# Kernel optimization log

Hardware: AMD Instinct MI355X
Metric: run time of the kernel (lower is better)

Reference implementation:

```python
import jax, jax.numpy as jnp
import numpy as np

N = 50000      # nodes
E = 800000     # edges (before self-loops)
F_IN = 128     # in_dim
H = 8          # heads
C = 16         # out_dim per head
NEG_SLOPE = 0.2
EPS = 1e-5


def setup_inputs() -> dict:
    key = jax.random.key(0)
    ks = jax.random.split(key, 8)
    x = jax.random.normal(ks[0], (N, F_IN), dtype=jnp.float32)
    edge_index = jax.random.randint(ks[1], (2, E), 0, N, dtype=jnp.int64)
    # GAT linear weight (xavier-ish scale), stored as [F_IN, H*C]
    W_gat = jax.random.normal(ks[2], (F_IN, H * C), dtype=jnp.float32) * 0.1
    att_src = jax.random.normal(ks[3], (H, C), dtype=jnp.float32) * 0.1
    att_dst = jax.random.normal(ks[4], (H, C), dtype=jnp.float32) * 0.1
    bias_gat = jnp.zeros((H * C,), dtype=jnp.float32)
    W_skip = jax.random.normal(ks[5], (F_IN, H * C), dtype=jnp.float32) * 0.1
    gamma = jnp.ones((H * C,), dtype=jnp.float32)
    beta = jnp.zeros((H * C,), dtype=jnp.float32)
    return {"x": x, "edge_index": edge_index, "W_gat": W_gat,
            "att_src": att_src, "att_dst": att_dst, "bias_gat": bias_gat,
            "W_skip": W_skip, "gamma": gamma, "beta": beta}


def reference(x, edge_index, W_gat, att_src, att_dst, bias_gat, W_skip, gamma, beta):
    # PyG GATConv default: add self-loops
    loop = jnp.arange(N, dtype=edge_index.dtype)
    src = jnp.concatenate([edge_index[0], loop])  # [E+N]
    dst = jnp.concatenate([edge_index[1], loop])  # [E+N]

    h = (x @ W_gat).reshape(N, H, C)              # [N,H,C]
    a_src = jnp.sum(h * att_src, axis=-1)          # [N,H]
    a_dst = jnp.sum(h * att_dst, axis=-1)          # [N,H]

    e = jax.nn.leaky_relu(a_src[src] + a_dst[dst], NEG_SLOPE)   # [E+N,H]
    # segment softmax over destination nodes
    e_max = jax.ops.segment_max(e, dst, num_segments=N)         # [N,H]
    e_exp = jnp.exp(e - e_max[dst])
    denom = jax.ops.segment_sum(e_exp, dst, num_segments=N)     # [N,H]
    alpha = e_exp / denom[dst]                                   # [E+N,H]

    msg = alpha[:, :, None] * h[src]                             # [E+N,H,C]
    gat_out = jax.ops.segment_sum(msg, dst, num_segments=N)     # [N,H,C]
    gat_out = gat_out.reshape(N, H * C) + bias_gat

    skip_out = x @ W_skip                                        # [N,H*C]
    z = gat_out + 0.1 * skip_out

    mu = jnp.mean(z, axis=-1, keepdims=True)
    var = jnp.mean((z - mu) ** 2, axis=-1, keepdims=True)
    z = (z - mu) * jax.lax.rsqrt(var + EPS) * gamma + beta
    return jax.nn.elu(z)  # dropout is identity in eval mode
```

## Files before the change

### kernel.cpp

```cpp
#include <hip/hip_runtime.h>
#include <hip/hip_bf16.h>

#define N_NODES 50000
#define N_EDGES 800000
#define F_IN    128
#define HC      128
#define NR      8
#define RSZ     6250
#define NCH     32
#define CHSZ    25000
#define NP      50048

#define LOG2E   1.4426950408889634f

typedef __attribute__((ext_vector_type(8))) short bf16x8;
typedef __attribute__((ext_vector_type(4))) float f32x4;

__device__ __forceinline__ float bf2f(unsigned int u16) {
    return __uint_as_float(u16 << 16);
}
__device__ __forceinline__ unsigned int f2bf2(float lo, float hi) {
    unsigned int r;
    asm("v_cvt_pk_bf16_f32 %0, %1, %2" : "=v"(r) : "v"(lo), "v"(hi));
    return r;
}
__device__ __forceinline__ float exp2_hw(float x) {
    float r;
    asm("v_exp_f32 %0, %1" : "=v"(r) : "v"(x));
    return r;
}

__device__ __forceinline__ void linear_block(
    int lin, int tid, int* smem,
    const float* __restrict__ x, const unsigned short* __restrict__ Bfrag,
    const float* __restrict__ att_s, const float* __restrict__ att_d,
    const float* __restrict__ bias,
    unsigned short* __restrict__ h_bf, unsigned int* __restrict__ z0b,
    float* __restrict__ a_src, float* __restrict__ a_dst)
{
    unsigned short* sA = (unsigned short*)smem;
    const int lane = tid & 63;
    const int w = tid >> 6;
    const int nbase = lin * 64;

#pragma unroll
    for (int it = 0; it < 4; it++) {
        const int p = it * 256 + tid;
        const int node = p >> 4;
        const int kg = p & 15;
        const int gn = nbase + node;
        float v[8];
        if (gn < N_NODES) {
            float4 u0 = *(const float4*)(x + (size_t)gn * F_IN + kg * 8);
            float4 u1 = *(const float4*)(x + (size_t)gn * F_IN + kg * 8 + 4);
            v[0] = u0.x; v[1] = u0.y; v[2] = u0.z; v[3] = u0.w;
            v[4] = u1.x; v[5] = u1.y; v[6] = u1.z; v[7] = u1.w;
        } else {
#pragma unroll
            for (int j = 0; j < 8; j++) v[j] = 0.f;
        }
        const int mt = node >> 4, lm = node & 15;
        const int kq = kg >> 2, quad = kg & 3;
        uint4 pk;
        pk.x = f2bf2(v[0], v[1]);
        pk.y = f2bf2(v[2], v[3]);
        pk.z = f2bf2(v[4], v[5]);
        pk.w = f2bf2(v[6], v[7]);
        *(uint4*)(sA + ((size_t)((mt * 4 + kq) * 64 + quad * 16 + lm)) * 8) = pk;
    }
    __syncthreads();

    const bf16x8* Bf = (const bf16x8*)Bfrag;
    f32x4 acc[4][4];
#pragma unroll
    for (int mt = 0; mt < 4; mt++)
#pragma unroll
        for (int nt = 0; nt < 4; nt++)
            acc[mt][nt] = (f32x4){0.f, 0.f, 0.f, 0.f};

#pragma unroll
    for (int kq = 0; kq < 4; kq++) {
        bf16x8 aF[4], bF[4];
#pragma unroll
        for (int nt = 0; nt < 4; nt++)
            bF[nt] = Bf[(size_t)(((w * 4 + nt) * 4 + kq) * 64 + lane)];
#pragma unroll
        for (int mt = 0; mt < 4; mt++)
            aF[mt] = *(const bf16x8*)(sA + ((size_t)((mt * 4 + kq) * 64 + lane)) * 8);
#pragma unroll
        for (int mt = 0; mt < 4; mt++)
#pragma unroll
            for (int nt = 0; nt < 4; nt++)
                acc[mt][nt] = __builtin_amdgcn_mfma_f32_16x16x32_bf16(
                    aF[mt], bF[nt], acc[mt][nt], 0, 0, 0);
    }

    __syncthreads();

    const int row4 = (lane >> 4) * 4;
    const int cl = lane & 15;
    unsigned int* hls = (unsigned int*)smem;

    if (w < 2) {
#pragma unroll
        for (int mt = 0; mt < 4; mt++) {
#pragma unroll
            for (int nt = 0; nt < 4; nt++) {
                const int cc = w * 64 + nt * 16 + cl;
                f32x4 d = acc[mt][nt];
#pragma unroll
                for (int rr = 0; rr < 4; rr++) {
                    const float oth = __shfl_xor(d[rr], 1);
                    const unsigned int pk = f2bf2(d[rr], oth);
                    if ((cl & 1) == 0) {
                        const int nl = mt * 16 + row4 + rr;
                        hls[nl * 68 + (cc >> 1)] = pk;
                    }
                }
            }
        }
    } else {
#pragma unroll
        for (int mt = 0; mt < 4; mt++) {
#pragma unroll
            for (int nt = 0; nt < 4; nt++) {
                const int cz = (w - 2) * 64 + nt * 16 + cl;
                f32x4 d = acc[mt][nt];
                const float bv = bias[cz];
#pragma unroll
                for (int rr = 0; rr < 4; rr++) {
                    const int gn = nbase + mt * 16 + row4 + rr;
                    const float val = 0.1f * d[rr] + bv;
                    const float oth = __shfl_xor(val, 1);
                    const unsigned int pk = f2bf2(val, oth);
                    if ((cl & 1) == 0 && gn < N_NODES)
                        z0b[(size_t)gn * 64 + (cz >> 1)] = pk;
                }
            }
        }
    }
    __syncthreads();

    {
        const int row = tid >> 2, q = tid & 3;
        const int gn = nbase + row;
        if (gn < N_NODES) {
            const unsigned int* hr = hls + row * 68 + q * 16;
            uint4 v0 = *(const uint4*)(hr);
            uint4 v1 = *(const uint4*)(hr + 4);
            uint4 v2 = *(const uint4*)(hr + 8);
            uint4 v3 = *(const uint4*)(hr + 12);
            uint4* hout = (uint4*)((unsigned int*)h_bf + (size_t)gn * 64 + q * 16);
            hout[0] = v0; hout[1] = v1; hout[2] = v2; hout[3] = v3;

            const unsigned int u[16] = {v0.x, v0.y, v0.z, v0.w,
                                        v1.x, v1.y, v1.z, v1.w,
                                        v2.x, v2.y, v2.z, v2.w,
                                        v3.x, v3.y, v3.z, v3.w};
            const int c0 = q * 32;
            const float4* as4 = (const float4*)(att_s + c0);
            const float4* ad4 = (const float4*)(att_d + c0);
            float ds0 = 0.f, dd0 = 0.f, ds1 = 0.f, dd1 = 0.f;
#pragma unroll
            for (int j = 0; j < 4; j++) {
                const float4 sa = as4[j], da = ad4[j];
                float l0 = bf2f(u[2 * j] & 0xffffu),     h0v = bf2f(u[2 * j] >> 16);
                float l1 = bf2f(u[2 * j + 1] & 0xffffu), h1v = bf2f(u[2 * j + 1] >> 16);
                ds0 += l0 * sa.x + h0v * sa.y + l1 * sa.z + h1v * sa.w;
                dd0 += l0 * da.x + h0v * da.y + l1 * da.z + h1v * da.w;
                const float4 sb = as4[4 + j], db = ad4[4 + j];
                float l2 = bf2f(u[8 + 2 * j] & 0xffffu),     h2v = bf2f(u[8 + 2 * j] >> 16);
                float l3 = bf2f(u[8 + 2 * j + 1] & 0xffffu), h3v = bf2f(u[8 + 2 * j + 1] >> 16);
                ds1 += l2 * sb.x + h2v * sb.y + l3 * sb.z + h3v * sb.w;
                dd1 += l2 * db.x + h2v * db.y + l3 * db.z + h3v * db.w;
            }
            const int hh = 2 * q;
            a_src[gn * 8 + hh]     = ds0 * LOG2E;
            a_src[gn * 8 + hh + 1] = ds1 * LOG2E;
            a_dst[gn * 8 + hh]     = dd0 * LOG2E;
            a_dst[gn * 8 + hh + 1] = dd1 * LOG2E;
        }
    }
}

__global__ __launch_bounds__(256) void k_pack(
    const float* __restrict__ Wg, const float* __restrict__ Ws,
    unsigned short* __restrict__ Bfrag)
{
    const int g = blockIdx.x * 256 + threadIdx.x;
    if (g < 4096) {
        const int lane = g & 63;
        const int kq = (g >> 6) & 3;
        const int nt = g >> 8;
        const int cc = nt * 16 + (lane & 15);
        const int kbase = kq * 32 + (lane >> 4) * 8;
        const float* Wsel = (cc < 128) ? (Wg + cc) : (Ws + cc - 128);
        unsigned int pk[4];
#pragma unroll
        for (int p = 0; p < 4; p++) {
            const float v0 = Wsel[(size_t)(kbase + 2 * p) * HC];
            const float v1 = Wsel[(size_t)(kbase + 2 * p + 1) * HC];
            pk[p] = f2bf2(v0, v1);
        }
        *(uint4*)(Bfrag + (size_t)g * 8) = make_uint4(pk[0], pk[1], pk[2], pk[3]);
    }
}

__global__ __launch_bounds__(256) void k_hl(
    const int* __restrict__ dst, int* __restrict__ part,
    const float* __restrict__ x, const unsigned short* __restrict__ Bfrag,
    const float* __restrict__ att_s, const float* __restrict__ att_d,
    const float* __restrict__ bias,
    unsigned short* __restrict__ h_bf, unsigned int* __restrict__ z0b,
    float* __restrict__ a_src, float* __restrict__ a_dst)
{
    __shared__ __align__(16) int smem[RSZ];
    const int bid = blockIdx.x;
    const int tid = threadIdx.x;
    if (bid < 256) {
        const int r = bid & 7, c = bid >> 3;
        const int nb = r * RSZ;
        for (int i = tid; i < RSZ; i += 256) smem[i] = 0;
        __syncthreads();
        const int4* d4 = (const int4*)(dst + c * CHSZ);
        for (int i = tid; i < CHSZ / 4; i += 256) {
            const int4 v = d4[i];
            int b;
            b = v.x - nb; if ((unsigned)b < (unsigned)RSZ) atomicAdd(&smem[b], 1);
            b = v.y - nb; if ((unsigned)b < (unsigned)RSZ) atomicAdd(&smem[b], 1);
            b = v.z - nb; if ((unsigned)b < (unsigned)RSZ) atomicAdd(&smem[b], 1);
            b = v.w - nb; if ((unsigned)b < (unsigned)RSZ) atomicAdd(&smem[b], 1);
        }
        __syncthreads();
        for (int i = tid; i < RSZ; i += 256)
            part[(size_t)c * NP + nb + i] = smem[i];
        return;
    }
    linear_block(bid - 256, tid, smem, x, Bfrag, att_s, att_d, bias,
                 h_bf, z0b, a_src, a_dst);
}

__global__ __launch_bounds__(256) void k_sl(
    int* __restrict__ part, int* __restrict__ counts,
    int* __restrict__ row_start, int* __restrict__ bsum,
    const float* __restrict__ x, const unsigned short* __restrict__ Bfrag,
    const float* __restrict__ att_s, const float* __restrict__ att_d,
    const float* __restrict__ bias,
    unsigned short* __restrict__ h_bf, unsigned int* __restrict__ z0b,
    float* __restrict__ a_src, float* __restrict__ a_dst)
{
    __shared__ __align__(16) int smem[RSZ];
    const int bid = blockIdx.x;
    const int tid = threadIdx.x;
    if (bid < 49) {
        int* s = smem;
        const int base = bid * 1024 + tid * 4;
        int v[4]; int t = 0;
#pragma unroll
        for (int j = 0; j < 4; j++) {
            const int idx = base + j;
            if (idx < N_NODES) {
                int run = 0;
#pragma unroll
                for (int c = 0; c < NCH; c++) {
                    int* p = part + (size_t)c * NP + idx;
                    const int q = *p;
                    *p = run;
                    run += q;
                }
                counts[idx] = run;
                v[j] = run + 1;
            } else v[j] = 0;
            t += v[j];
        }
        s[tid] = t;
        __syncthreads();
        for (int off = 1; off < 256; off <<= 1) {
            int add = (tid >= off) ? s[tid - off] : 0;
            __syncthreads();
            s[tid] += add;
            __syncthreads();
        }
        int excl = s[tid] - t;
#pragma unroll
        for (int j = 0; j < 4; j++) {
            const int idx = base + j;
            if (idx < N_NODES) row_start[idx] = excl;
            excl += v[j];
        }
        if (tid == 255) bsum[bid] = s[255];
        return;
    }
    linear_block(260 + (bid - 49), tid, smem, x, Bfrag, att_s, att_d, bias,
                 h_bf, z0b, a_src, a_dst);
}

__global__ __launch_bounds__(256) void k_lf(
    const int* __restrict__ src, const int* __restrict__ dst,
    const int* __restrict__ row_start, const int* __restrict__ part,
    const int* __restrict__ bsum, const int* __restrict__ counts,
    int* __restrict__ row_fin, int* __restrict__ csr,
    const float* __restrict__ x, const unsigned short* __restrict__ Bfrag,
    const float* __restrict__ att_s, const float* __restrict__ att_d,
    const float* __restrict__ bias,
    unsigned short* __restrict__ h_bf, unsigned int* __restrict__ z0b,
    float* __restrict__ a_src, float* __restrict__ a_dst)
{
    __shared__ __align__(16) int smem[RSZ];
    __shared__ int pbsum[64];
    const int bid = blockIdx.x;
    const int tid = threadIdx.x;
    int lin;
    if (bid < 512) {
        const int c = bid >> 4, pos = bid & 15;
        if (pos < 8) {
            const int r = pos;
            const int nb = r * RSZ;
            if (tid < 64) {
                const int val = (tid < 49) ? bsum[tid] : 0;
                int v = val;
#pragma unroll
                for (int off = 1; off < 64; off <<= 1) {
                    const int u = __shfl_up(v, off);
                    if (tid >= off) v += u;
                }
                pbsum[tid] = v - val;
            }
            __syncthreads();
            if (c == 0) {
                for (int b = tid; b < RSZ; b += 256) {
                    const int idx = nb + b;
                    const int rsf = row_start[idx] + pbsum[idx >> 10];
                    smem[b] = rsf + part[(size_t)c * NP + idx];
                    row_fin[idx] = rsf;
                    csr[rsf + counts[idx]] = idx;
                }
            } else {
                for (int b = tid; b < RSZ; b += 256) {
                    const int idx = nb + b;
                    smem[b] = row_start[idx] + pbsum[idx >> 10]
                            + part[(size_t)c * NP + idx];
                }
            }
            __syncthreads();
            const int4* d4 = (const int4*)(dst + c * CHSZ);
            const int4* s4 = (const int4*)(src + c * CHSZ);
            for (int i = tid; i < CHSZ / 4; i += 256) {
                const int4 dv = d4[i];
                const int4 sv = s4[i];
                int b;
                b = dv.x - nb; if ((unsigned)b < (unsigned)RSZ) csr[atomicAdd(&smem[b], 1)] = sv.x;
                b = dv.y - nb; if ((unsigned)b < (unsigned)RSZ) csr[atomicAdd(&smem[b], 1)] = sv.y;
                b = dv.z - nb; if ((unsigned)b < (unsigned)RSZ) csr[atomicAdd(&smem[b], 1)] = sv.z;
                b = dv.w - nb; if ((unsigned)b < (unsigned)RSZ) csr[atomicAdd(&smem[b], 1)] = sv.w;
            }
            return;
        }
        lin = 521 + c * 8 + (pos - 8);
    } else {
        lin = 777 + (bid - 512);
    }
    linear_block(lin, tid, smem, x, Bfrag, att_s, att_d, bias,
                 h_bf, z0b, a_src, a_dst);
}

__global__ __launch_bounds__(256) void k_agg(
    const unsigned int* __restrict__ h32,
    const unsigned int* __restrict__ z0b,
    const float* __restrict__ a_src, const float* __restrict__ a_dst,
    const int* __restrict__ row_fin, const int* __restrict__ counts,
    const int* __restrict__ csr,
    const float* __restrict__ gamma, const float* __restrict__ beta,
    float* __restrict__ out)
{
    const int tid = threadIdx.x;
    const int lane = tid & 63;
    const int n = blockIdx.x * 4 + (tid >> 6);
    const int head = lane >> 3;

    const float adn = a_dst[n * 8 + head];
    const int rs  = __builtin_amdgcn_readfirstlane(row_fin[n]);
    const int cnt = __builtin_amdgcn_readfirstlane(counts[n]) + 1;

    const char* h8 = (const char*)h32;
    const char* a8 = (const char*)a_src;
    const unsigned int hoff = (unsigned)(lane << 2);
    const unsigned int aoff = (unsigned)(head << 2);

    float d_acc = 0.f, a0 = 0.f, a1 = 0.f;
    const int nfull16 = cnt & ~15;
    int i = 0;
    for (; i < nfull16; i += 16) {
        int s[16]; float ae[16]; unsigned int hp[16];
#pragma unroll
        for (int j = 0; j < 16; j++) s[j] = csr[rs + i + j];
#pragma unroll
        for (int j = 0; j < 16; j++)
            ae[j] = *(const float*)(a8 + ((unsigned)(s[j] << 5) | aoff));
#pragma unroll
        for (int j = 0; j < 16; j++)
            hp[j] = *(const unsigned int*)(h8 + ((unsigned)(s[j] << 8) | hoff));
#pragma unroll
        for (int j = 0; j < 16; j++) {
            float e = ae[j] + adn;
            e = fmaxf(e, 0.2f * e);
            const float wgt = exp2_hw(e);
            d_acc += wgt;
            a0 += wgt * bf2f(hp[j] & 0xffffu);
            a1 += wgt * bf2f(hp[j] >> 16);
        }
    }
    if (i + 8 <= cnt) {
        int s[8]; float ae[8]; unsigned int hp[8];
#pragma unroll
        for (int j = 0; j < 8; j++) s[j] = csr[rs + i + j];
#pragma unroll
        for (int j = 0; j < 8; j++)
            ae[j] = *(const float*)(a8 + ((unsigned)(s[j] << 5) | aoff));
#pragma unroll
        for (int j = 0; j < 8; j++)
            hp[j] = *(const unsigned int*)(h8 + ((unsigned)(s[j] << 8) | hoff));
#pragma unroll
        for (int j = 0; j < 8; j++) {
            float e = ae[j] + adn;
            e = fmaxf(e, 0.2f * e);
            const float wgt = exp2_hw(e);
            d_acc += wgt;
            a0 += wgt * bf2f(hp[j] & 0xffffu);
            a1 += wgt * bf2f(hp[j] >> 16);
        }
        i += 8;
    }
    if (i < cnt) {
        int s[8]; float ae[8], mk[8]; unsigned int hp[8];
#pragma unroll
        for (int j = 0; j < 8; j++) {
            const int e = i + j;
            const int ec = (e < cnt) ? e : (cnt - 1);
            mk[j] = (e < cnt) ? 1.f : 0.f;
            s[j] = csr[rs + ec];
        }
#pragma unroll
        for (int j = 0; j < 8; j++)
            ae[j] = *(const float*)(a8 + ((unsigned)(s[j] << 5) | aoff));
#pragma unroll
        for (int j = 0; j < 8; j++)
            hp[j] = *(const unsigned int*)(h8 + ((unsigned)(s[j] << 8) | hoff));
#pragma unroll
        for (int j = 0; j < 8; j++) {
            float e = ae[j] + adn;
            e = fmaxf(e, 0.2f * e);
            const float wgt = exp2_hw(e) * mk[j];
            d_acc += wgt;
            a0 += wgt * bf2f(hp[j] & 0xffffu);
            a1 += wgt * bf2f(hp[j] >> 16);
        }
    }
    const float inv = 1.0f / d_acc;
    const unsigned int zp = z0b[(size_t)n * 64 + lane];
    float y0 = a0 * inv + bf2f(zp & 0xffffu);
    float y1 = a1 * inv + bf2f(zp >> 16);

    float ss = y0 + y1;
#pragma unroll
    for (int off = 1; off < 64; off <<= 1) ss += __shfl_xor(ss, off);
    const float mu = ss * (1.0f / 128.0f);
    const float d0 = y0 - mu, d1 = y1 - mu;
    float vs = d0 * d0 + d1 * d1;
#pragma unroll
    for (int off = 1; off < 64; off <<= 1) vs += __shfl_xor(vs, off);
    const float rstd = rsqrtf(vs * (1.0f / 128.0f) + 1e-5f);

    const float2 gv = *(const float2*)(gamma + lane * 2);
    const float2 bv = *(const float2*)(beta + lane * 2);
    float o0 = d0 * rstd * gv.x + bv.x;
    float o1 = d1 * rstd * gv.y + bv.y;
    o0 = (o0 > 0.f) ? o0 : (__expf(o0) - 1.0f);
    o1 = (o1 > 0.f) ? o1 : (__expf(o1) - 1.0f);

    *(float2*)(out + (size_t)n * HC + lane * 2) = make_float2(o0, o1);
}

extern "C" void kernel_launch(void* const* d_in, const int* in_sizes, int n_in,
                              void* d_out, int out_size, void* d_ws, size_t ws_size,
                              hipStream_t stream) {
    const float* x   = (const float*)d_in[0];
    const int*   ei  = (const int*)d_in[1];
    const float* Wg  = (const float*)d_in[2];
    const float* as_ = (const float*)d_in[3];
    const float* ad_ = (const float*)d_in[4];
    const float* bg  = (const float*)d_in[5];
    const float* Wsk = (const float*)d_in[6];
    const float* gm  = (const float*)d_in[7];
    const float* bt  = (const float*)d_in[8];
    float* out = (float*)d_out;

    char* wsb = (char*)d_ws;
    unsigned short* h_bf  = (unsigned short*)wsb;
    unsigned int*   z0b   = (unsigned int*)(wsb + 12800000);
    float*          a_src = (float*)(wsb + 25600000);
    float*          a_dst = (float*)(wsb + 27200000);
    unsigned short* Bfrag = (unsigned short*)(wsb + 28800000);
    int*   counts = (int*)(wsb + 28865536);
    int*   row_st = (int*)(wsb + 29065728);
    int*   bsum   = (int*)(wsb + 29265920);
    int*   csr    = (int*)(wsb + 29266944);
    int*   part   = (int*)(wsb + 32666944);
    int*   row_fin= (int*)(wsb + 39073088);

    const int* src = ei;
    const int* dst = ei + N_EDGES;

    k_pack <<<16, 256, 0, stream>>>(Wg, Wsk, Bfrag);
    k_hl   <<<516, 256, 0, stream>>>(dst, part, x, Bfrag, as_, ad_, bg,
                                     h_bf, z0b, a_src, a_dst);
    k_sl   <<<310, 256, 0, stream>>>(part, counts, row_st, bsum,
                                     x, Bfrag, as_, ad_, bg,
                                     h_bf, z0b, a_src, a_dst);
    k_lf   <<<517, 256, 0, stream>>>(src, dst, row_st, part, bsum, counts,
                                     row_fin, csr,
                                     x, Bfrag, as_, ad_, bg,
                                     h_bf, z0b, a_src, a_dst);
    k_agg  <<<N_NODES / 4, 256, 0, stream>>>((const unsigned int*)h_bf, z0b,
                                             a_src, a_dst, row_fin, counts, csr,
                                             gm, bt, out);
}
```

Measured before the change: 202.1 us.

## Split wavefront into two half-waves each gathering alternate edges with 8-byte loads

The aggregation kernel now splits each 64-lane wavefront into two 32-lane halves. Each half processes alternate incoming edges, with every lane loading 4 bf16 features (8 bytes) per edge, and the halves are combined with a single cross-half shuffle before the layernorm. This halves the number of serial edge iterations per node and widens each gather load, aiming to raise memory-level parallelism in the latency-bound gather. The cost is duplicated a_src loads per half, a partial-final-batch mask per half, and half the lanes idling at the final store.

Result: no change. 201.8 us (-0.2%).

```diff
diff --git a/kernel.cpp b/kernel.cpp
--- a/kernel.cpp
+++ b/kernel.cpp
@@ -375,8 +375,10 @@
 {
     const int tid = threadIdx.x;
     const int lane = tid & 63;
+    const int half = lane >> 5;
+    const int q = lane & 31;
+    const int head = q >> 2;
     const int n = blockIdx.x * 4 + (tid >> 6);
-    const int head = lane >> 3;
 
     const float adn = a_dst[n * 8 + head];
     const int rs  = __builtin_amdgcn_readfirstlane(row_fin[n]);
@@ -384,101 +386,112 @@
 
     const char* h8 = (const char*)h32;
     const char* a8 = (const char*)a_src;
-    const unsigned int hoff = (unsigned)(lane << 2);
+    const unsigned int hoff = (unsigned)(q << 3);
     const unsigned int aoff = (unsigned)(head << 2);
 
-    float d_acc = 0.f, a0 = 0.f, a1 = 0.f;
-    const int nfull16 = cnt & ~15;
+    float d_acc = 0.f;
+    float acc0 = 0.f, acc1 = 0.f, acc2 = 0.f, acc3 = 0.f;
+
     int i = 0;
-    for (; i < nfull16; i += 16) {
-        int s[16]; float ae[16]; unsigned int hp[16];
-#pragma unroll
-        for (int j = 0; j < 16; j++) s[j] = csr[rs + i + j];
-#pragma unroll
-        for (int j = 0; j < 16; j++)
-            ae[j] = *(const float*)(a8 + ((unsigned)(s[j] << 5) | aoff));
-#pragma unroll
-        for (int j = 0; j < 16; j++)
-            hp[j] = *(const unsigned int*)(h8 + ((unsigned)(s[j] << 8) | hoff));
-#pragma unroll
-        for (int j = 0; j < 16; j++) {
-            float e = ae[j] + adn;
+    for (; i + 16 <= cnt; i += 16) {
+        unsigned ho[8], ao[8];
+#pragma unroll
+        for (int p = 0; p < 8; p++) {
+            const int s0 = csr[rs + i + 2 * p];
+            const int s1 = csr[rs + i + 2 * p + 1];
+            const int sv = half ? s1 : s0;
+            ho[p] = ((unsigned)sv << 8) | hoff;
+            ao[p] = ((unsigned)sv << 5) | aoff;
+        }
+        float ae[8]; uint2 hp[8];
+#pragma unroll
+        for (int p = 0; p < 8; p++)
+            ae[p] = *(const float*)(a8 + ao[p]);
+#pragma unroll
+        for (int p = 0; p < 8; p++)
+            hp[p] = *(const uint2*)(h8 + ho[p]);
+#pragma unroll
+        for (int p = 0; p < 8; p++) {
+            float e = ae[p] + adn;
             e = fmaxf(e, 0.2f * e);
             const float wgt = exp2_hw(e);
             d_acc += wgt;
-            a0 += wgt * bf2f(hp[j] & 0xffffu);
-            a1 += wgt * bf2f(hp[j] >> 16);
-        }
-    }
-    if (i + 8 <= cnt) {
-        int s[8]; float ae[8]; unsigned int hp[8];
-#pragma unroll
-        for (int j = 0; j < 8; j++) s[j] = csr[rs + i + j];
-#pragma unroll
-        for (int j = 0; j < 8; j++)
-            ae[j] = *(const float*)(a8 + ((unsigned)(s[j] << 5) | aoff));
-#pragma unroll
-        for (int j = 0; j < 8; j++)
-            hp[j] = *(const unsigned int*)(h8 + ((unsigned)(s[j] << 8) | hoff));
-#pragma unroll
-        for (int j = 0; j < 8; j++) {
-            float e = ae[j] + adn;
+            acc0 += wgt * bf2f(hp[p].x & 0xffffu);
+            acc1 += wgt * bf2f(hp[p].x >> 16);
+            acc2 += wgt * bf2f(hp[p].y & 0xffffu);
+            acc3 += wgt * bf2f(hp[p].y >> 16);
+        }
+    }
+    for (; i < cnt; i += 8) {
+        unsigned ho[4], ao[4]; float mk[4];
+#pragma unroll
+        for (int p = 0; p < 4; p++) {
+            const int e0 = i + 2 * p;
+            const int i0 = (e0     < cnt) ? e0     : (cnt - 1);
+            const int i1 = (e0 + 1 < cnt) ? e0 + 1 : (cnt - 1);
+            const int s0 = csr[rs + i0];
+            const int s1 = csr[rs + i1];
+            const int sv = half ? s1 : s0;
+            mk[p] = ((e0 + half) < cnt) ? 1.f : 0.f;
+            ho[p] = ((unsigned)sv << 8) | hoff;
+            ao[p] = ((unsigned)sv << 5) | aoff;
+        }
+        float ae[4]; uint2 hp[4];
+#pragma unroll
+        for (int p = 0; p < 4; p++)
+            ae[p] = *(const float*)(a8 + ao[p]);
+#pragma unroll
+        for (int p = 0; p < 4; p++)
+            hp[p] = *(const uint2*)(h8 + ho[p]);
+#pragma unroll
+        for (int p = 0; p < 4; p++) {
+            float e = ae[p] + adn;
             e = fmaxf(e, 0.2f * e);
-            const float wgt = exp2_hw(e);
+            const float wgt = exp2_hw(e) * mk[p];
             d_acc += wgt;
-            a0 += wgt * bf2f(hp[j] & 0xffffu);
-            a1 += wgt * bf2f(hp[j] >> 16);
-        }
-        i += 8;
-    }
-    if (i < cnt) {
-        int s[8]; float ae[8], mk[8]; unsigned int hp[8];
-#pragma unroll
-        for (int j = 0; j < 8; j++) {
-            const int e = i + j;
-            const int ec = (e < cnt) ? e : (cnt - 1);
-            mk[j] = (e < cnt) ? 1.f : 0.f;
-            s[j] = csr[rs + ec];
-        }
-#pragma unroll
-        for (int j = 0; j < 8; j++)
-            ae[j] = *(const float*)(a8 + ((unsigned)(s[j] << 5) | aoff));
-#pragma unroll
-        for (int j = 0; j < 8; j++)
-            hp[j] = *(const unsigned int*)(h8 + ((unsigned)(s[j] << 8) | hoff));
-#pragma unroll
-        for (int j = 0; j < 8; j++) {
-            float e = ae[j] + adn;
-            e = fmaxf(e, 0.2f * e);
-            const float wgt = exp2_hw(e) * mk[j];
-            d_acc += wgt;
-            a0 += wgt * bf2f(hp[j] & 0xffffu);
-            a1 += wgt * bf2f(hp[j] >> 16);
-        }
-    }
+            acc0 += wgt * bf2f(hp[p].x & 0xffffu);
+            acc1 += wgt * bf2f(hp[p].x >> 16);
+            acc2 += wgt * bf2f(hp[p].y & 0xffffu);
+            acc3 += wgt * bf2f(hp[p].y >> 16);
+        }
+    }
+
+    d_acc += __shfl_xor(d_acc, 32);
+    acc0 += __shfl_xor(acc0, 32);
+    acc1 += __shfl_xor(acc1, 32);
+    acc2 += __shfl_xor(acc2, 32);
+    acc3 += __shfl_xor(acc3, 32);
+
     const float inv = 1.0f / d_acc;
-    const unsigned int zp = z0b[(size_t)n * 64 + lane];
-    float y0 = a0 * inv + bf2f(zp & 0xffffu);
-    float y1 = a1 * inv + bf2f(zp >> 16);
-
-    float ss = y0 + y1;
-#pragma unroll
-    for (int off = 1; off < 64; off <<= 1) ss += __shfl_xor(ss, off);
+    const uint2 zp = *(const uint2*)((const char*)z0b + (size_t)n * 256 + (q << 3));
+    float y0 = acc0 * inv + bf2f(zp.x & 0xffffu);
+    float y1 = acc1 * inv + bf2f(zp.x >> 16);
+    float y2 = acc2 * inv + bf2f(zp.y & 0xffffu);
+    float y3 = acc3 * inv + bf2f(zp.y >> 16);
+
+    float ss = y0 + y1 + y2 + y3;
+#pragma unroll
+    for (int off = 1; off < 32; off <<= 1) ss += __shfl_xor(ss, off);
     const float mu = ss * (1.0f / 128.0f);
-    const float d0 = y0 - mu, d1 = y1 - mu;
-    float vs = d0 * d0 + d1 * d1;
-#pragma unroll
-    for (int off = 1; off < 64; off <<= 1) vs += __shfl_xor(vs, off);
+    const float d0 = y0 - mu, d1 = y1 - mu, d2 = y2 - mu, d3 = y3 - mu;
+    float vs = d0 * d0 + d1 * d1 + d2 * d2 + d3 * d3;
+#pragma unroll
+    for (int off = 1; off < 32; off <<= 1) vs += __shfl_xor(vs, off);
     const float rstd = rsqrtf(vs * (1.0f / 128.0f) + 1e-5f);
 
-    const float2 gv = *(const float2*)(gamma + lane * 2);
-    const float2 bv = *(const float2*)(beta + lane * 2);
+    const float4 gv = *(const float4*)(gamma + q * 4);
+    const float4 bv = *(const float4*)(beta + q * 4);
     float o0 = d0 * rstd * gv.x + bv.x;
     float o1 = d1 * rstd * gv.y + bv.y;
+    float o2 = d2 * rstd * gv.z + bv.z;
+    float o3 = d3 * rstd * gv.w + bv.w;
     o0 = (o0 > 0.f) ? o0 : (__expf(o0) - 1.0f);
     o1 = (o1 > 0.f) ? o1 : (__expf(o1) - 1.0f);
-
-    *(float2*)(out + (size_t)n * HC + lane * 2) = make_float2(o0, o1);
+    o2 = (o2 > 0.f) ? o2 : (__expf(o2) - 1.0f);
+    o3 = (o3 > 0.f) ? o3 : (__expf(o3) - 1.0f);
+
+    if (half == 0)
+        *(float4*)(out + (size_t)n * HC + q * 4) = make_float4(o0, o1, o2, o3);
 }
 
 extern "C" void kernel_launch(void* const* d_in, const int* in_sizes, int n_in,
```
